# Optimization experiments

Measured on AMD Instinct MI355X. Metric: run time of the kernel, lower is better.

Reference implementation:

```python
import jax, jax.numpy as jnp
import numpy as np

S = 7; B = 2; C = 20
IMG_W = 448.0; IMG_H = 448.0
CONF_THRES = 0.5; NMS_THRES = 0.5; IOU_THRES = [0.5]
N = S * S  # 49 boxes per image (one responsible box per cell)
BATCH = 4096


def setup_inputs() -> dict:
    key = jax.random.key(0)
    k1, k2 = jax.random.split(key)
    target = jax.random.uniform(k1, (BATCH, S, S, B * 5 + C), dtype=jnp.float32)
    output = jax.random.normal(k2, (BATCH, S, S, B * 5 + C), dtype=jnp.float32)
    return {"target": target, "output": output}


def _decode(coords):
    # coords: [b,S,S,4] cell-normalized (x,y,w,h) -> xyxy pixel boxes [b,S,S,4]
    gw, gh = IMG_W / S, IMG_H / S
    jx = jnp.arange(S, dtype=coords.dtype)[None, None, :, None]  # column index -> cx
    iy = jnp.arange(S, dtype=coords.dtype)[None, :, None, None]  # row index    -> cy
    cx = (coords[..., 0:1] + jx) * gw
    cy = (coords[..., 1:2] + iy) * gh
    w = coords[..., 2:3] * IMG_W
    h = coords[..., 3:4] * IMG_H
    return jnp.concatenate([cx - w / 2, cy - h / 2, cx + w / 2, cy + h / 2], axis=-1)


def _pairwise_iou(a, b):
    # a: [M,4], b: [K,4] xyxy -> [M,K] IoU (torchvision box_iou semantics)
    lt = jnp.maximum(a[:, None, :2], b[None, :, :2])
    rb = jnp.minimum(a[:, None, 2:], b[None, :, 2:])
    wh = jnp.clip(rb - lt, 0.0)
    inter = wh[..., 0] * wh[..., 1]
    area_a = (a[:, 2] - a[:, 0]) * (a[:, 3] - a[:, 1])
    area_b = (b[:, 2] - b[:, 0]) * (b[:, 3] - b[:, 1])
    return inter / (area_a[:, None] + area_b[None, :] - inter)


def _per_image(ob, oc, ocls, tb, tconf, tcls):
    # Sort preds by conf desc (batched_nms returns score-descending keep order)
    order = jnp.argsort(-oc)
    b_s, c_s, k_s = ob[order], oc[order], ocls[order]
    # class-aware greedy NMS over the 49 boxes
    iou_pp = _pairwise_iou(b_s, b_s)
    sup = (iou_pp > NMS_THRES) & (k_s[:, None] == k_s[None, :])
    idx = jnp.arange(N)
    def nms_body(suppressed, i):
        active = ~suppressed[i]
        suppressed = suppressed | (active & sup[i] & (idx > i))
        return suppressed, active
    _, keep = jax.lax.scan(nms_body, jnp.zeros((N,), bool), idx)
    valid_p = keep & (c_s > CONF_THRES)
    valid_g = tconf > CONF_THRES
    # best same-class GT per pred (max_iou starts at 0 in original; -1 sentinel OK since thr>0)
    cand = (k_s[:, None] == tcls[None, :]) & valid_g[None, :]
    miou = jnp.where(cand, _pairwise_iou(b_s, tb), -1.0)
    return k_s, valid_p, jnp.max(miou, axis=-1), jnp.argmax(miou, axis=-1), valid_g


def _match(mx, best, valid_p, thr):
    # greedy TP/FP assignment over preds in conf-desc order, per image
    def body(matched, i):
        hit = valid_p[i] & (mx[i] > thr) & (~matched[best[i]])
        matched = matched.at[best[i]].set(matched[best[i]] | hit)
        return matched, hit
    _, tp = jax.lax.scan(body, jnp.zeros((N,), bool), jnp.arange(N))
    return tp


def reference(target, output):
    D = B * 5 + C
    target = target.reshape(-1, S, S, D)
    output = jax.nn.sigmoid(output.reshape(-1, S, S, D))
    bsz = output.shape[0]
    # ground-truth decode
    tconf = target[..., 4].reshape(bsz, N)
    tcls = jnp.argmax(target[..., B * 5:], axis=-1).reshape(bsz, N)
    tb = _decode(target[..., 0:4]).reshape(bsz, N, 4)
    # prediction decode: responsible box = max-conf box per cell
    confs = jnp.stack([output[..., b * 5 + 4] for b in range(B)], axis=-1)  # [b,S,S,B]
    oc = jnp.max(confs, axis=-1).reshape(bsz, N)
    resp = jnp.argmax(confs, axis=-1)
    coords = sum((resp == b)[..., None] * output[..., b * 5:b * 5 + 4] for b in range(B))
    ob = _decode(coords).reshape(bsz, N, 4)
    ocls = jnp.argmax(output[..., B * 5:], axis=-1).reshape(bsz, N)

    k_s, valid_p, mx, best, valid_g = jax.vmap(_per_image)(ob, oc, ocls, tb, tconf, tcls)

    # flatten in (image, conf-desc) order == original pred_boxes order
    cls_f = k_s.reshape(-1)
    vp_f = valid_p.reshape(-1)
    gt_count = jax.ops.segment_sum(valid_g.reshape(-1).astype(jnp.float32),
                                   tcls.reshape(-1), num_segments=C)  # [C]
    mask = (cls_f[None, :] == jnp.arange(C)[:, None]) & vp_f[None, :]  # [C, bsz*N]

    aps = []
    for thr in IOU_THRES:
        tp = jax.vmap(_match, in_axes=(0, 0, 0, None))(mx, best, valid_p, thr)
        tp = tp.reshape(-1).astype(jnp.float32)
        # masked entries keep cum values constant -> contribute 0 to trapz
        tpc = jnp.cumsum(jnp.where(mask, tp[None, :], 0.0), axis=1)
        fpc = jnp.cumsum(jnp.where(mask, 1.0 - tp[None, :], 0.0), axis=1)
        recall = tpc / (gt_count[:, None] + 1e-6)
        prec = tpc / (tpc + fpc + 1e-6)
        r = jnp.concatenate([jnp.zeros((C, 1), recall.dtype), recall], axis=1)
        p = jnp.concatenate([jnp.ones((C, 1), prec.dtype), prec], axis=1)
        ap = jnp.sum((r[:, 1:] - r[:, :-1]) * (p[:, 1:] + p[:, :-1]) * 0.5, axis=1)
        has = gt_count > 0  # classes with no GT are skipped in original
        n_has = jnp.maximum(jnp.sum(has.astype(jnp.float32)), 1.0)
        aps.append(jnp.sum(jnp.where(has, ap, 0.0)) / n_has)
    return sum(aps) / len(aps)
```

## Files before the change

kernel.cpp:

```cpp
#include <hip/hip_runtime.h>
#include <stdint.h>

#pragma clang fp contract(off)

#define NCELL 49
#define NCLS  20
#define NSEG  16

struct Box { float x1, y1, x2, y2; };

__device__ __forceinline__ float sigmoid_ref(float x) {
#pragma clang fp contract(off)
  float z = expf(-fabsf(x));
  float num = (x >= 0.0f) ? 1.0f : z;
  return num / (1.0f + z);
}

__device__ __forceinline__ float iou_box(Box a, Box b) {
#pragma clang fp contract(off)
  float lx = fmaxf(a.x1, b.x1);
  float ly = fmaxf(a.y1, b.y1);
  float rx = fminf(a.x2, b.x2);
  float ry = fminf(a.y2, b.y2);
  float w = fmaxf(rx - lx, 0.0f);
  float h = fmaxf(ry - ly, 0.0f);
  float inter = w * h;
  float aa = (a.x2 - a.x1) * (a.y2 - a.y1);
  float ab = (b.x2 - b.x1) * (b.y2 - b.y1);
  return inter / (aa + ab - inter);
}

__device__ __forceinline__ bool iou_gt_half(Box a, Box b) {
#pragma clang fp contract(off)
  float lx = fmaxf(a.x1, b.x1);
  float ly = fmaxf(a.y1, b.y1);
  float rx = fminf(a.x2, b.x2);
  float ry = fminf(a.y2, b.y2);
  float w = fmaxf(rx - lx, 0.0f);
  float h = fmaxf(ry - ly, 0.0f);
  float inter = w * h;
  float aa = (a.x2 - a.x1) * (a.y2 - a.y1);
  float ab = (b.x2 - b.x1) * (b.y2 - b.y1);
  float u = aa + ab - inter;
  return inter > 0.5f * u;
}

__device__ __forceinline__ unsigned mbcnt64(unsigned long long m) {
  return __builtin_amdgcn_mbcnt_hi((unsigned)(m >> 32),
         __builtin_amdgcn_mbcnt_lo((unsigned)m, 0u));
}
#define WSYNC() __builtin_amdgcn_wave_barrier()

__global__ __launch_bounds__(128) void k_per_image(
    const float* __restrict__ target, const float* __restrict__ output,
    uint8_t* __restrict__ entries, unsigned* __restrict__ gtseg,
    unsigned* __restrict__ totals, int batch, int segimg)
{
#pragma clang fp contract(off)
  __shared__ float4   pbox [2][64];
  __shared__ int2     pcc  [2][64];
  __shared__ float4   gboxC[2][64];
  __shared__ int      gorig[2][64];
  __shared__ float    ctab [2][64];
  __shared__ int      claim[2][64];
  __shared__ unsigned phist[2][NCLS];

  int tid = threadIdx.x;
  int lane = tid & 63;
  int wv = tid >> 6;
  int img = blockIdx.x * 2 + wv;
  if (img >= batch) return;
  bool a = (lane < NCELL);
  int seg = img / segimg;

  if (lane < NCLS) phist[wv][lane] = 0u;
  claim[wv][lane] = 64;

  float fjx = (float)(lane % 7), fiy = (float)(lane / 7);

  float ov[30], tv[30];
  if (a) {
    const float2* O2 = (const float2*)(output + (size_t)img * 1470 + lane * 30);
    const float2* T2 = (const float2*)(target + (size_t)img * 1470 + lane * 30);
#pragma unroll
    for (int i = 0; i < 15; ++i) { float2 o = O2[i]; ov[2*i] = o.x; ov[2*i+1] = o.y; }
#pragma unroll
    for (int i = 0; i < 15; ++i) { float2 t = T2[i]; tv[2*i] = t.x; tv[2*i+1] = t.y; }
  } else {
#pragma unroll
    for (int i = 0; i < 30; ++i) { ov[i] = 0.0f; tv[i] = 0.0f; }
  }

  {
    float myc = -1.0f; int myk = 0; float px1 = 0, py1 = 0, px2 = 0, py2 = 0;
    if (a) {
      float x4 = ov[4], x9 = ov[9];
      float xm = fmaxf(x4, x9);
      float xc = ov[10], xr = -3.0e38f; int kk = 0;
#pragma unroll
      for (int c = 1; c < NCLS; ++c) {
        float v = ov[10 + c];
        bool gt = v > xc;
        float nr = gt ? xc : fmaxf(xr, v);
        kk = gt ? c : kk;
        xc = gt ? v : xc;
        xr = nr;
      }
      bool slowK = (xc - xr) < fmaxf(1e-5f, 4e-6f * exp2f(xc * 1.44269504f));
      bool slowR = fabsf(x4 - x9) < fmaxf(1e-5f, 4e-6f * exp2f(xm * 1.44269504f));
      int resp = (x9 > x4) ? 1 : 0;
      myc = sigmoid_ref(xm);
      myk = kk;
      if (slowK || slowR) {
        float s0 = sigmoid_ref(x4);
        float s1 = sigmoid_ref(x9);
        myc = fmaxf(s0, s1);
        resp = (s1 > s0) ? 1 : 0;
        float obv = sigmoid_ref(ov[10]); myk = 0;
#pragma unroll
        for (int c = 1; c < NCLS; ++c) {
          float v = sigmoid_ref(ov[10 + c]);
          if (v > obv) { obv = v; myk = c; }
        }
      }
      float bx = resp ? ov[5] : ov[0];
      float by = resp ? ov[6] : ov[1];
      float bw = resp ? ov[7] : ov[2];
      float bh = resp ? ov[8] : ov[3];
      float x  = sigmoid_ref(bx);
      float y  = sigmoid_ref(by);
      float ww = sigmoid_ref(bw);
      float hh = sigmoid_ref(bh);
      float cx = (x + fjx) * 64.0f, cy = (y + fiy) * 64.0f;
      float W = ww * 448.0f, H = hh * 448.0f;
      px1 = cx - W * 0.5f; py1 = cy - H * 0.5f;
      px2 = cx + W * 0.5f; py2 = cy + H * 0.5f;
    }
    ctab[wv][lane] = myc;
    WSYNC();
    int r = 0;
#pragma unroll
    for (int j = 0; j < NCELL; ++j) {
      float cj = ctab[wv][j];
      r += (cj > myc) || (cj == myc && j < lane);
    }
    r = a ? r : lane;
    pbox[wv][r] = make_float4(px1, py1, px2, py2);
    pcc [wv][r] = make_int2(myk, __float_as_int(myc));
  }

  int mystartR = 0, myendR = 0;
  unsigned gcnt_mine = 0;
  int gclsv = 0; bool gval = false;
  float4 gb4;
  {
    float tbv = tv[10];
#pragma unroll
    for (int c = 1; c < NCLS; ++c) { float v = tv[10 + c]; if (v > tbv) { tbv = v; gclsv = c; } }
    gval = a && (tv[4] > 0.5f);
    float cx = (tv[0] + fjx) * 64.0f, cy = (tv[1] + fiy) * 64.0f;
    float w2 = tv[2] * 448.0f, h2 = tv[3] * 448.0f;
    gb4 = make_float4(cx - w2 * 0.5f, cy - h2 * 0.5f,
                      cx + w2 * 0.5f, cy + h2 * 0.5f);
  }

  WSYNC();
  float4 sb4 = pbox[wv][lane];
  int2 cc = pcc[wv][lane];
  Box myS; myS.x1 = sb4.x; myS.y1 = sb4.y; myS.x2 = sb4.z; myS.y2 = sb4.w;
  int scls = cc.x; float sconf = __int_as_float(cc.y);

  {
    int base = 0, mypos = -1;
#pragma unroll
    for (int c = 0; c < NCLS; ++c) {
      unsigned long long mc = __ballot(gval && (gclsv == c));
      int cnt = (int)__popcll(mc);
      if (scls == c) { mystartR = base; myendR = base + cnt; }
      if (gval && gclsv == c) mypos = base + (int)mbcnt64(mc);
      if (lane == c) gcnt_mine = (unsigned)cnt;
      base += cnt;
    }
    if (mypos >= 0) {
      gboxC[wv][mypos] = gb4;
      gorig[wv][mypos] = lane;
    }
    if (lane < NCLS && gcnt_mine) atomicAdd(&gtseg[seg * 32 + lane], gcnt_mine);
  }
  if (!a) { mystartR = 0; myendR = 0; }
  WSYNC();

  float mx = -1.0f; int best = 0;
  for (int g = mystartR; g < myendR; ++g) {
    float4 b4 = gboxC[wv][g];
    int og = gorig[wv][g];
    Box bg; bg.x1 = b4.x; bg.y1 = b4.y; bg.x2 = b4.z; bg.y2 = b4.w;
    float v = iou_box(myS, bg);
    bool upd = (v > mx);
    mx = upd ? v : mx;
    best = upd ? og : best;
  }

  unsigned long long row = 0;
#pragma unroll 4
  for (int t = 1; t <= 24; ++t) {
    int jr = lane + t;
    bool wrapped = (jr >= 49);
    int j = wrapped ? jr - 49 : jr;
    float4 b4 = pbox[wv][j];
    int kj = pcc[wv][j].x;
    Box bj; bj.x1 = b4.x; bj.y1 = b4.y; bj.x2 = b4.z; bj.y2 = b4.w;
    bool s = a && (scls == kj) && iou_gt_half(myS, bj);
    row |= (s && !wrapped) ? (1ull << (jr & 63)) : 0ull;
    unsigned long long m2 = __ballot(s && wrapped);
    int idx = lane + 49 - t;
    unsigned long long bit = (m2 >> (idx & 63)) & 1ull;
    row |= (idx < 49) ? (bit << (idx & 63)) : 0ull;
  }
  unsigned long long anyrow = __ballot(row != 0ull);
  unsigned supbit = 0u;
  while (anyrow) {
    int i = (int)__builtin_ctzll(anyrow);
    anyrow &= anyrow - 1;
    unsigned long long ri = __shfl(row, i, 64);
    unsigned si = __shfl(supbit, i, 64);
    supbit |= (!si && ((ri >> lane) & 1ull)) ? 1u : 0u;
  }
  bool vp = a && (supbit == 0u) && (sconf > 0.5f);

  bool elig = vp && (mx > 0.5f);
  if (elig) atomicMin(&claim[wv][best], lane);
  WSYNC();
  bool hit = elig && (claim[wv][best] == lane);

  if (a) {
    entries[(size_t)img * NCELL + lane] =
        (uint8_t)(scls | (vp ? 32 : 0) | (hit ? 64 : 0));
  }

  unsigned add = (vp ? 0x10000u : 0u) | (hit ? 1u : 0u);
  if (a && add) atomicAdd(&phist[wv][scls], add);
  WSYNC();
  if (lane < NCLS) {
    unsigned pkt = phist[wv][lane];
    if (pkt) atomicAdd(&totals[seg * 32 + lane], pkt);
  }
}

__device__ __forceinline__ unsigned match_mask(unsigned w, unsigned wantx4) {
  unsigned y = (w & 0x3f3f3f3fu) ^ wantx4;
  return ~(y + 0x7f7f7f7fu) & 0x80808080u;
}

__device__ __forceinline__ uint4 load_tile(const uint8_t* entries, int e, int e1, int ne) {
  uint4 w4 = make_uint4(0, 0, 0, 0);
  if (e < e1) {
    int p = e << 4;
    if (p + 16 <= ne) {
      w4 = *(const uint4*)(entries + p);
    } else {
      unsigned ws[4] = {0, 0, 0, 0};
      for (int k = 0; k < ne - p; ++k)
        ws[k >> 2] |= ((unsigned)entries[p + k]) << (8 * (k & 3));
      w4.x = ws[0]; w4.y = ws[1]; w4.z = ws[2]; w4.w = ws[3];
    }
  }
  return w4;
}

__global__ __launch_bounds__(256) void k_apB(
    const uint8_t* __restrict__ entries, const unsigned* __restrict__ totals,
    const unsigned* __restrict__ gtseg, double* __restrict__ partials,
    unsigned* __restrict__ counter, float* __restrict__ out,
    int ne, int segimg)
{
#pragma clang fp contract(off)
  int c = blockIdx.x / NSEG, s = blockIdx.x % NSEG;
  int tid = threadIdx.x, wid = tid >> 6, lane = tid & 63;
  unsigned gtc = 0;
#pragma unroll
  for (int s2 = 0; s2 < NSEG; ++s2) gtc += gtseg[s2 * 32 + c];
  float g2 = (float)gtc + 1e-6f;
  unsigned wantx4 = (32u + (unsigned)c) * 0x01010101u;

  int nel = (ne + 15) >> 4;
  int segel = segimg * NCELL / 16;
  int se0 = s * segel; if (se0 > nel) se0 = nel;
  int se1 = se0 + segel; if (se1 > nel) se1 = nel;
  int elw = (se1 > se0) ? ((se1 - se0 + 3) >> 2) : 0;
  int e0 = se0 + wid * elw; if (e0 > se1) e0 = se1;
  int e1 = e0 + elw; if (e1 > se1) e1 = se1;
  int ntile = (e1 > e0) ? ((e1 - e0 + 63) >> 6) : 0;

  unsigned long long pk = 0;
  if (lane < s) {
    unsigned t2 = totals[lane * 32 + c];
    pk = ((unsigned long long)(t2 >> 16) << 32) | (unsigned long long)(t2 & 0xffffu);
  }
#pragma unroll
  for (int d = 1; d < 64; d <<= 1) pk += __shfl_xor(pk, d, 64);
  unsigned Jrun = (unsigned)(pk >> 32), Trun = (unsigned)(pk & 0xffffffffull);

  unsigned mv = 0, mt = 0;
  for (int t = 0; t < ntile; ++t) {
    uint4 w4 = load_tile(entries, e0 + t * 64 + lane, e1, ne);
    unsigned wsv[4] = {w4.x, w4.y, w4.z, w4.w};
#pragma unroll
    for (int q = 0; q < 4; ++q) {
      unsigned m = match_mask(wsv[q], wantx4);
      mv += __popc(m);
      mt += __popc(m & (wsv[q] << 1));
    }
  }
  unsigned long long tot = ((unsigned long long)mv << 32) | (unsigned long long)mt;
#pragma unroll
  for (int d = 1; d < 64; d <<= 1) tot += __shfl_xor(tot, d, 64);
  __shared__ unsigned long long wt[4];
  __shared__ double wacc[4];
  __shared__ int islast;
  __shared__ float apf_s[NCLS];
  __shared__ unsigned ghas_s[NCLS];
  if (lane == 0) wt[wid] = tot;
  __syncthreads();
  for (int w2 = 0; w2 < wid; ++w2) {
    Jrun += (unsigned)(wt[w2] >> 32);
    Trun += (unsigned)(wt[w2] & 0xffffffffull);
  }

  double acc = 0.0;
  for (int t = 0; t < ntile; ++t) {
    int e = e0 + t * 64 + lane;
    int p = e << 4;
    uint4 w4 = load_tile(entries, e, e1, ne);
    unsigned wsv[4] = {w4.x, w4.y, w4.z, w4.w};
    unsigned mm[4], tm[4];
    unsigned cv = 0, ct = 0;
#pragma unroll
    for (int q = 0; q < 4; ++q) {
      unsigned m = match_mask(wsv[q], wantx4);
      mm[q] = m; tm[q] = m & (wsv[q] << 1);
      cv += __popc(m); ct += __popc(tm[q]);
    }
    unsigned jexcl = 0, texcl = 0, jtt = 0, ttt = 0;
#pragma unroll
    for (int b = 0; b < 5; ++b) {
      unsigned long long mj = __ballot(((cv >> b) & 1u) != 0u);
      unsigned long long mk = __ballot(((ct >> b) & 1u) != 0u);
      jexcl += mbcnt64(mj) << b;
      texcl += mbcnt64(mk) << b;
      jtt   += (unsigned)__popcll(mj) << b;
      ttt   += (unsigned)__popcll(mk) << b;
    }
    unsigned jr = Jrun + jexcl;
    unsigned tr = Trun + texcl;
#pragma unroll
    for (int q = 0; q < 4; ++q) {
      unsigned m = mm[q];
      while (m) {
        unsigned bit = (unsigned)__builtin_ctz(m);
        m &= m - 1;
        ++jr;
        if (tm[q] & (1u << bit)) {
          ++tr;
          int pos = p + 4 * q + (int)(bit >> 3);
          float ft = (float)tr, fj = (float)jr;
          float r_cur  = ft / g2;
          float r_prev = (ft - 1.0f) / g2;
          float p_cur  = ft / (fj + 1e-6f);
          float p_prev = (pos == 0) ? 1.0f
                                    : (ft - 1.0f) / ((fj - 1.0f) + 1e-6f);
          acc += (double)((r_cur - r_prev) * (p_cur + p_prev) * 0.5f);
        }
      }
    }
    Jrun += jtt;
    Trun += ttt;
  }

  for (int d = 32; d > 0; d >>= 1) acc += __shfl_down(acc, d, 64);
  if (lane == 0) wacc[wid] = acc;
  __syncthreads();
  if (tid == 0) {
    double bp = wacc[0] + wacc[1] + wacc[2] + wacc[3];
    __hip_atomic_store(&partials[blockIdx.x], bp,
                       __ATOMIC_RELEASE, __HIP_MEMORY_SCOPE_AGENT);
    unsigned prev = __hip_atomic_fetch_add(counter, 1u,
                       __ATOMIC_ACQ_REL, __HIP_MEMORY_SCOPE_AGENT);
    islast = (prev == (unsigned)(NCLS * NSEG - 1)) ? 1 : 0;
  }
  __syncthreads();
  if (islast) {
    if (tid < NCLS) {
      double d2 = 0.0;
#pragma unroll
      for (int s2 = 0; s2 < NSEG; ++s2)
        d2 += __hip_atomic_load(&partials[tid * NSEG + s2],
                                __ATOMIC_ACQUIRE, __HIP_MEMORY_SCOPE_AGENT);
      apf_s[tid] = (float)d2;
      unsigned gc = 0;
#pragma unroll
      for (int s2 = 0; s2 < NSEG; ++s2) gc += gtseg[s2 * 32 + tid];
      ghas_s[tid] = gc;
    }
    __syncthreads();
    if (tid == 0) {
      float sf = 0.0f, nf = 0.0f;
      for (int cc = 0; cc < NCLS; ++cc)
        if (ghas_s[cc] > 0) { sf += apf_s[cc]; nf += 1.0f; }
      out[0] = sf / fmaxf(nf, 1.0f);
    }
  }
}

extern "C" void kernel_launch(void* const* d_in, const int* in_sizes, int n_in,
                              void* d_out, int out_size, void* d_ws, size_t ws_size,
                              hipStream_t stream) {
  const float* target = (const float*)d_in[0];
  const float* output = (const float*)d_in[1];
  int batch = in_sizes[0] / (NCELL * 30);
  int ne = batch * NCELL;
  int segimg = (((batch + NSEG - 1) / NSEG) + 15) & ~15;

  uint8_t*  entries  = (uint8_t*)d_ws;
  size_t offA = ((size_t)ne + 255) & ~(size_t)255;
  unsigned* totals   = (unsigned*)((char*)d_ws + offA);
  unsigned* gtseg    = (unsigned*)((char*)d_ws + offA + 2048);
  unsigned* counter  = (unsigned*)((char*)d_ws + offA + 4096);
  double*   partials = (double*)((char*)d_ws + offA + 4352);

  (void)hipMemsetAsync((char*)d_ws + offA, 0, 4352, stream);
  k_per_image<<<(batch + 1) / 2, 128, 0, stream>>>(
      target, output, entries, gtseg, totals, batch, segimg);
  k_apB<<<NCLS * NSEG, 256, 0, stream>>>(
      entries, totals, gtseg, partials, counter, (float*)d_out, ne, segimg);
}
```

Baseline: 116.1 us.

## Add single-pass 1024-thread AP kernel processing one tile per thread

Adds a variant of the AP accumulation kernel that uses 1024-thread blocks, so each segment's tiles are covered in one pass with one tile per lane. This removes the per-wave looping and carried running counts of the 256-thread version. It is used when a segment has at most 1024 tiles, and the original kernel remains as a fallback. Larger blocks can reduce occupancy flexibility and add block-wide synchronisation cost.

```diff
diff --git a/kernel.cpp b/kernel.cpp
--- a/kernel.cpp
+++ b/kernel.cpp
@@ -268,6 +268,136 @@
   return w4;
 }
 
+__global__ __launch_bounds__(1024) void k_apB_fast(
+    const uint8_t* __restrict__ entries, const unsigned* __restrict__ totals,
+    const unsigned* __restrict__ gtseg, double* __restrict__ partials,
+    unsigned* __restrict__ counter, float* __restrict__ out,
+    int ne, int segimg)
+{
+#pragma clang fp contract(off)
+  int c = blockIdx.x / NSEG, s = blockIdx.x % NSEG;
+  int tid = threadIdx.x, wid = tid >> 6, lane = tid & 63;
+  unsigned gtc = 0;
+#pragma unroll
+  for (int s2 = 0; s2 < NSEG; ++s2) gtc += gtseg[s2 * 32 + c];
+  float g2 = (float)gtc + 1e-6f;
+  unsigned wantx4 = (32u + (unsigned)c) * 0x01010101u;
+
+  int nel = (ne + 15) >> 4;
+  int segel = segimg * NCELL / 16;
+  int se0 = s * segel; if (se0 > nel) se0 = nel;
+  int se1 = se0 + segel; if (se1 > nel) se1 = nel;
+  int elw = (se1 > se0) ? ((se1 - se0 + 15) >> 4) : 0;
+  int e0 = se0 + wid * elw; if (e0 > se1) e0 = se1;
+  int e1 = e0 + elw; if (e1 > se1) e1 = se1;
+
+  unsigned long long pk = 0;
+  if (lane < s) {
+    unsigned t2 = totals[lane * 32 + c];
+    pk = ((unsigned long long)(t2 >> 16) << 32) | (unsigned long long)(t2 & 0xffffu);
+  }
+#pragma unroll
+  for (int d = 1; d < 64; d <<= 1) pk += __shfl_xor(pk, d, 64);
+  unsigned Jrun = (unsigned)(pk >> 32), Trun = (unsigned)(pk & 0xffffffffull);
+
+  int e = e0 + lane;
+  int p = e << 4;
+  uint4 w4 = load_tile(entries, e, e1, ne);
+  unsigned wsv[4] = {w4.x, w4.y, w4.z, w4.w};
+  unsigned mm[4], tm[4];
+  unsigned cv = 0, ct = 0;
+#pragma unroll
+  for (int q = 0; q < 4; ++q) {
+    unsigned m = match_mask(wsv[q], wantx4);
+    mm[q] = m; tm[q] = m & (wsv[q] << 1);
+    cv += __popc(m); ct += __popc(tm[q]);
+  }
+
+  unsigned long long tot = ((unsigned long long)cv << 32) | (unsigned long long)ct;
+#pragma unroll
+  for (int d = 1; d < 64; d <<= 1) tot += __shfl_xor(tot, d, 64);
+  __shared__ unsigned long long wt[16];
+  __shared__ double wacc[16];
+  __shared__ int islast;
+  __shared__ float apf_s[NCLS];
+  __shared__ unsigned ghas_s[NCLS];
+  if (lane == 0) wt[wid] = tot;
+  __syncthreads();
+  for (int w2 = 0; w2 < wid; ++w2) {
+    Jrun += (unsigned)(wt[w2] >> 32);
+    Trun += (unsigned)(wt[w2] & 0xffffffffull);
+  }
+
+  unsigned jexcl = 0, texcl = 0;
+#pragma unroll
+  for (int b = 0; b < 5; ++b) {
+    unsigned long long mj = __ballot(((cv >> b) & 1u) != 0u);
+    unsigned long long mk = __ballot(((ct >> b) & 1u) != 0u);
+    jexcl += mbcnt64(mj) << b;
+    texcl += mbcnt64(mk) << b;
+  }
+  unsigned jr = Jrun + jexcl;
+  unsigned tr = Trun + texcl;
+
+  double acc = 0.0;
+#pragma unroll
+  for (int q = 0; q < 4; ++q) {
+    unsigned m = mm[q];
+    while (m) {
+      unsigned bit = (unsigned)__builtin_ctz(m);
+      m &= m - 1;
+      ++jr;
+      if (tm[q] & (1u << bit)) {
+        ++tr;
+        int pos = p + 4 * q + (int)(bit >> 3);
+        float ft = (float)tr, fj = (float)jr;
+        float r_cur  = ft / g2;
+        float r_prev = (ft - 1.0f) / g2;
+        float p_cur  = ft / (fj + 1e-6f);
+        float p_prev = (pos == 0) ? 1.0f
+                                  : (ft - 1.0f) / ((fj - 1.0f) + 1e-6f);
+        acc += (double)((r_cur - r_prev) * (p_cur + p_prev) * 0.5f);
+      }
+    }
+  }
+
+  for (int d = 32; d > 0; d >>= 1) acc += __shfl_down(acc, d, 64);
+  if (lane == 0) wacc[wid] = acc;
+  __syncthreads();
+  if (tid == 0) {
+    double bp = 0.0;
+#pragma unroll
+    for (int w2 = 0; w2 < 16; ++w2) bp += wacc[w2];
+    __hip_atomic_store(&partials[blockIdx.x], bp,
+                       __ATOMIC_RELEASE, __HIP_MEMORY_SCOPE_AGENT);
+    unsigned prev = __hip_atomic_fetch_add(counter, 1u,
+                       __ATOMIC_ACQ_REL, __HIP_MEMORY_SCOPE_AGENT);
+    islast = (prev == (unsigned)(NCLS * NSEG - 1)) ? 1 : 0;
+  }
+  __syncthreads();
+  if (islast) {
+    if (tid < NCLS) {
+      double d2 = 0.0;
+#pragma unroll
+      for (int s2 = 0; s2 < NSEG; ++s2)
+        d2 += __hip_atomic_load(&partials[tid * NSEG + s2],
+                                __ATOMIC_ACQUIRE, __HIP_MEMORY_SCOPE_AGENT);
+      apf_s[tid] = (float)d2;
+      unsigned gc = 0;
+#pragma unroll
+      for (int s2 = 0; s2 < NSEG; ++s2) gc += gtseg[s2 * 32 + tid];
+      ghas_s[tid] = gc;
+    }
+    __syncthreads();
+    if (tid == 0) {
+      float sf = 0.0f, nf = 0.0f;
+      for (int cc = 0; cc < NCLS; ++cc)
+        if (ghas_s[cc] > 0) { sf += apf_s[cc]; nf += 1.0f; }
+      out[0] = sf / fmaxf(nf, 1.0f);
+    }
+  }
+}
+
 __global__ __launch_bounds__(256) void k_apB(
     const uint8_t* __restrict__ entries, const unsigned* __restrict__ totals,
     const unsigned* __restrict__ gtseg, double* __restrict__ partials,
@@ -431,6 +561,12 @@
   (void)hipMemsetAsync((char*)d_ws + offA, 0, 4352, stream);
   k_per_image<<<(batch + 1) / 2, 128, 0, stream>>>(
       target, output, entries, gtseg, totals, batch, segimg);
-  k_apB<<<NCLS * NSEG, 256, 0, stream>>>(
-      entries, totals, gtseg, partials, counter, (float*)d_out, ne, segimg);
-}
+  int segel = segimg * NCELL / 16;
+  if (segel <= 1024) {
+    k_apB_fast<<<NCLS * NSEG, 1024, 0, stream>>>(
+        entries, totals, gtseg, partials, counter, (float*)d_out, ne, segimg);
+  } else {
+    k_apB<<<NCLS * NSEG, 256, 0, stream>>>(
+        entries, totals, gtseg, partials, counter, (float*)d_out, ne, segimg);
+  }
+}
```

After: 116.4 us. No clear change (+0.2%).
